# Kernel tuning notes

Hardware: AMD Instinct MI355X
Metric: run time of the kernel (lower is better)

## Reference

```python
import jax, jax.numpy as jnp
import numpy as np

BS, NC, CN, DN = 8, 1024, 64, 64
GH, GW = 32, 32
ALPHA, BPC = 4, 4
G = 8
IN_LO, IN_HI = 0, ALPHA
OUT_LO, OUT_HI = ALPHA, 2 * ALPHA
B_LO, B_HI = 2 * ALPHA, 2 * ALPHA + BPC
HS, HM, HMOD = 256, 256, 128
MOD_IN = 3 * DN + 2 + BPC
MOD_OUT = DN + BPC


def setup_inputs():
    key = jax.random.key(0)
    ks = iter(jax.random.split(key, 40))
    def nrm(shape, s=0.05):
        return jax.random.normal(next(ks), shape, dtype=jnp.float32) * s
    return {
        "x": nrm((BS, NC * DN), 1.0),
        "h": nrm((BS, NC, CN, DN), 0.01),
        "msg": nrm((BS, NC, CN, DN), 0.1),
        "W": nrm((BS, NC, CN, CN), 0.1),
        "decay_logit": jnp.zeros((BS, NC, CN), jnp.float32),
        "cell_context": jnp.zeros((BS, NC, DN), jnp.float32),
        "border_gate_logit": jnp.zeros((BS, NC, BPC), jnp.float32),
        "neuron_id": nrm((NC, CN, DN), 0.02),
        "state_w1": nrm((HS, 2 * DN)), "state_b1": jnp.zeros((HS,), jnp.float32),
        "state_gs1": jnp.ones((G, HS), jnp.float32), "state_gb1": jnp.zeros((G, HS), jnp.float32),
        "state_w2": nrm((DN, HS)), "state_b2": jnp.zeros((DN,), jnp.float32),
        "state_gs2": jnp.ones((G, DN), jnp.float32), "state_gb2": jnp.zeros((G, DN), jnp.float32),
        "msg_w1": nrm((HM, DN)), "msg_b1": jnp.zeros((HM,), jnp.float32),
        "msg_gs1": jnp.ones((G, HM), jnp.float32), "msg_gb1": jnp.zeros((G, HM), jnp.float32),
        "msg_w2": nrm((DN, HM)), "msg_b2": jnp.zeros((DN,), jnp.float32),
        "msg_gs2": jnp.ones((G, DN), jnp.float32), "msg_gb2": jnp.zeros((G, DN), jnp.float32),
        "inject_w": nrm((G, ALPHA * DN, DN)), "inject_b": jnp.zeros((G, ALPHA * DN), jnp.float32),
        "mod_w1": nrm((NC, MOD_IN, HMOD)), "mod_b1": jnp.zeros((NC, HMOD), jnp.float32),
        "mod_w2": nrm((NC, HMOD, MOD_OUT), 0.01), "mod_b2": jnp.zeros((NC, MOD_OUT), jnp.float32),
        "cell_to_group": jnp.arange(NC, dtype=jnp.int32) % G,
    }


def _grouped_mlp(x, c2g, w1, b1, gs1, gb1, w2, b2, gs2, gb2):
    # x: [B, NC, CN, F]; group-specific affine modulation after each linear.
    hid = jnp.einsum('bcnf,hf->bcnh', x, w1) + b1
    hid = jnp.tanh(hid * gs1[c2g][None, :, None, :] + gb1[c2g][None, :, None, :])
    out = jnp.einsum('bcnh,dh->bcnd', hid, w2) + b2
    return jnp.tanh(out * gs2[c2g][None, :, None, :] + gb2[c2g][None, :, None, :])


def reference(x, h, msg, W, decay_logit, cell_context, border_gate_logit, neuron_id,
              state_w1, state_b1, state_gs1, state_gb1, state_w2, state_b2, state_gs2, state_gb2,
              msg_w1, msg_b1, msg_gs1, msg_gb1, msg_w2, msg_b2, msg_gs2, msg_gb2,
              inject_w, inject_b, mod_w1, mod_b1, mod_w2, mod_b2, cell_to_group):
    c2g = cell_to_group
    # 1) dense message passing inside each cell: received = W @ msg
    received = jnp.einsum('bcnm,bcmd->bcnd', W, msg)
    # 2) inject external input into input ports (per-group orthogonal-init projections)
    cell_slice = x.reshape(BS, NC, DN)
    iw, ib = inject_w[c2g], inject_b[c2g]                      # [NC, alpha*DN, DN], [NC, alpha*DN]
    inject = jnp.einsum('bni,noi->bno', cell_slice, iw) + ib   # [BS, NC, alpha*DN]
    received = received.at[:, :, IN_LO:IN_HI].add(inject.reshape(BS, NC, ALPHA, DN))
    # 3) fixed geometric border exchange between neighboring grid cells
    border = msg[:, :, B_LO:B_HI].reshape(BS, GH, GW, BPC, DN)
    incoming = jnp.zeros_like(border)
    incoming = incoming.at[:, 1:, :, 0].set(border[:, :-1, :, 1])
    incoming = incoming.at[:, :-1, :, 1].set(border[:, 1:, :, 0])
    incoming = incoming.at[:, :, 1:, 2].set(border[:, :, :-1, 3])
    incoming = incoming.at[:, :, :-1, 3].set(border[:, :, 1:, 2])
    incoming = incoming.reshape(BS, NC, BPC, DN)
    border_gate = jax.nn.sigmoid(border_gate_logit)[..., None]
    received = received.at[:, :, B_LO:B_HI].add(border_gate * incoming)
    # 4) gated recurrent state update
    decay = jax.nn.sigmoid(decay_logit)[..., None]
    cand = _grouped_mlp(jnp.concatenate([received, h], axis=-1), c2g,
                        state_w1, state_b1, state_gs1, state_gb1,
                        state_w2, state_b2, state_gs2, state_gb2)
    h_new = decay * h + (1.0 - decay) * cand
    # 5) emit new messages (+ per-neuron identity embedding)
    msg_new = _grouped_mlp(h_new, c2g, msg_w1, msg_b1, msg_gs1, msg_gb1,
                           msg_w2, msg_b2, msg_gs2, msg_gb2) + neuron_id[None]
    # 6) readout from output ports
    readout = (msg_new[:, :, OUT_LO:OUT_HI].sum(axis=2) * (ALPHA ** -0.5)).reshape(BS, -1)
    # 7) per-cell modulation MLP (distinct weights per cell)
    h_mean = h_new.mean(axis=2)
    msg_mean = msg_new.mean(axis=2)
    W_row = jnp.abs(W).mean(axis=-1).mean(axis=2, keepdims=True)
    decay_mean = decay_logit.mean(axis=2, keepdims=True)
    feats = jnp.concatenate([h_mean, msg_mean, W_row, decay_mean,
                             cell_context, border_gate_logit], axis=-1)   # [BS, NC, MOD_IN]
    hid = jnp.tanh(jnp.einsum('bcf,cfh->bch', feats, mod_w1) + mod_b1)
    mod = jnp.einsum('bch,cho->bco', hid, mod_w2) + mod_b2                 # [BS, NC, MOD_OUT]
    cell_context_new = cell_context + mod[..., :DN]
    border_gate_logit_new = border_gate_logit + mod[..., DN:]
    return readout, h_new, msg_new, cell_context_new, border_gate_logit_new
```

## Files before the change

### kernel.cpp

```cpp
#include <hip/hip_runtime.h>

#define NCC 1024
#define MODIN 198
#define MODOUT 68
#define HMODL 128

typedef __attribute__((ext_vector_type(8))) short s8v;
typedef __attribute__((ext_vector_type(4))) float f4v;
typedef unsigned short ushort_t;
typedef unsigned int uint_t;

#define OFF_SW1 0
#define OFF_SW2 32768
#define OFF_MW1 49152
#define OFF_MW2 65536
#define FEATS_BYTE_OFF 262144

__device__ __forceinline__ float fast_tanh(float x) {
    const float e = __builtin_amdgcn_exp2f(x * 2.885390081777927f);
    const float r = __builtin_amdgcn_rcpf(e + 1.f);
    return fmaf(-2.f, r, 1.f);
}
__device__ __forceinline__ float fast_sigmoid(float x) {
    const float e = __builtin_amdgcn_exp2f(x * -1.4426950408889634f);
    return __builtin_amdgcn_rcpf(e + 1.f);
}
__device__ __forceinline__ ushort_t f2bf(float x) {
    uint_t u = __builtin_bit_cast(uint_t, x);
    u += 0x7FFFu + ((u >> 16) & 1u);
    return (ushort_t)(u >> 16);
}
__device__ __forceinline__ uint_t pk2(float a, float b) {
    return (uint_t)f2bf(a) | ((uint_t)f2bf(b) << 16);
}
#define SWZ(byteoff, row) ((byteoff) ^ (((row) & 7) << 4))

__global__ __launch_bounds__(256)
void mg_cvtw(const float* __restrict__ sw1, const float* __restrict__ sw2,
             const float* __restrict__ mw1, const float* __restrict__ mw2,
             ushort_t* __restrict__ o) {
    const int i = blockIdx.x * 256 + threadIdx.x;
    float v;
    if (i < 32768)      v = sw1[i];
    else if (i < 49152) v = sw2[i - 32768];
    else if (i < 65536) v = mw1[i - 49152];
    else                v = mw2[i - 65536];
    o[i] = f2bf(v);
}

__global__ __launch_bounds__(256, 4)
void mg_inject(const float* __restrict__ xp, const float* __restrict__ iw,
               const float* __restrict__ ibias, const int* __restrict__ c2g,
               float* __restrict__ injb) {
    const int c = blockIdx.x, t = threadIdx.x;
    const int g = c2g[c];
    __shared__ float s_x[8][64];
    for (int idx = t; idx < 512; idx += 256)
        s_x[idx >> 6][idx & 63] = xp[(size_t)(idx >> 6) * (NCC * 64) + c * 64 + (idx & 63)];
    __syncthreads();
    const float* wrow = iw + (size_t)g * 16384 + t * 64;
    float a0 = 0.f, a1 = 0.f, a2 = 0.f, a3 = 0.f, a4 = 0.f, a5 = 0.f, a6 = 0.f, a7 = 0.f;
    #pragma unroll
    for (int i = 0; i < 64; i += 4) {
        const float4 w4 = *(const float4*)(wrow + i);
        const float4 x0 = *(const float4*)&s_x[0][i];
        const float4 x1 = *(const float4*)&s_x[1][i];
        const float4 x2 = *(const float4*)&s_x[2][i];
        const float4 x3 = *(const float4*)&s_x[3][i];
        const float4 x4 = *(const float4*)&s_x[4][i];
        const float4 x5 = *(const float4*)&s_x[5][i];
        const float4 x6 = *(const float4*)&s_x[6][i];
        const float4 x7 = *(const float4*)&s_x[7][i];
        a0 = fmaf(w4.x, x0.x, a0); a0 = fmaf(w4.y, x0.y, a0); a0 = fmaf(w4.z, x0.z, a0); a0 = fmaf(w4.w, x0.w, a0);
        a1 = fmaf(w4.x, x1.x, a1); a1 = fmaf(w4.y, x1.y, a1); a1 = fmaf(w4.z, x1.z, a1); a1 = fmaf(w4.w, x1.w, a1);
        a2 = fmaf(w4.x, x2.x, a2); a2 = fmaf(w4.y, x2.y, a2); a2 = fmaf(w4.z, x2.z, a2); a2 = fmaf(w4.w, x2.w, a2);
        a3 = fmaf(w4.x, x3.x, a3); a3 = fmaf(w4.y, x3.y, a3); a3 = fmaf(w4.z, x3.z, a3); a3 = fmaf(w4.w, x3.w, a3);
        a4 = fmaf(w4.x, x4.x, a4); a4 = fmaf(w4.y, x4.y, a4); a4 = fmaf(w4.z, x4.z, a4); a4 = fmaf(w4.w, x4.w, a4);
        a5 = fmaf(w4.x, x5.x, a5); a5 = fmaf(w4.y, x5.y, a5); a5 = fmaf(w4.z, x5.z, a5); a5 = fmaf(w4.w, x5.w, a5);
        a6 = fmaf(w4.x, x6.x, a6); a6 = fmaf(w4.y, x6.y, a6); a6 = fmaf(w4.z, x6.z, a6); a6 = fmaf(w4.w, x6.w, a6);
        a7 = fmaf(w4.x, x7.x, a7); a7 = fmaf(w4.y, x7.y, a7); a7 = fmaf(w4.z, x7.z, a7); a7 = fmaf(w4.w, x7.w, a7);
    }
    const float bv = ibias[g * 256 + t];
    const float acc[8] = {a0, a1, a2, a3, a4, a5, a6, a7};
    #pragma unroll
    for (int b = 0; b < 8; b++)
        injb[((size_t)b * NCC + c) * 4096 + t] = acc[b] + bv;
}

__global__ __launch_bounds__(512, 4)
void mg_cell_kernel(
    const float* __restrict__ hp,   const float* __restrict__ msgp,
    const float* __restrict__ Wp,   const float* __restrict__ decayp,
    const float* __restrict__ bglp, const float* __restrict__ nidp,
    const float* __restrict__ sb1,  const float* __restrict__ sgs1,
    const float* __restrict__ sgb1, const float* __restrict__ sb2,
    const float* __restrict__ sgs2, const float* __restrict__ sgb2,
    const float* __restrict__ mb1,  const float* __restrict__ mgs1,
    const float* __restrict__ mgb1, const float* __restrict__ mb2,
    const float* __restrict__ mgs2, const float* __restrict__ mgb2,
    const int*   __restrict__ c2g,  const ushort_t* __restrict__ wb,
    float* __restrict__ out_read, float* __restrict__ out_h,
    float* __restrict__ out_msg,  float* __restrict__ wsf)
{
    const int t  = threadIdx.x;
    const int bc = blockIdx.x;
    const int b  = bc >> 10, c = bc & 1023;
    const int gh = c >> 5, gwc = c & 31;
    const int lane = t & 63, w = t >> 6;
    const int cl = lane & 15, q = lane >> 4;
    const int g  = c2g[c];
    const size_t tile = (size_t)bc * 4096;

    __shared__ ushort_t sHid[16384];
    __shared__ ushort_t sIn[8192];
    __shared__ float s_scr[256];
    __shared__ float s_dec[64];
    __shared__ float s_wsum[8];
    __shared__ float s_dsum;

    ushort_t* sW    = sHid;
    ushort_t* sMsgT = sHid + 4096;

    {
        const int n = t >> 3, m0 = (t & 7) * 8;
        const float* src = Wp + tile + n * 64 + m0;
        const float4 v0 = *(const float4*)(src);
        const float4 v1 = *(const float4*)(src + 4);
        float wsum = fabsf(v0.x) + fabsf(v0.y) + fabsf(v0.z) + fabsf(v0.w)
                   + fabsf(v1.x) + fabsf(v1.y) + fabsf(v1.z) + fabsf(v1.w);
        *(uint_t*)((char*)sW + SWZ(n * 128 + (m0 + 0) * 2, n)) = pk2(v0.x, v0.y);
        *(uint_t*)((char*)sW + SWZ(n * 128 + (m0 + 2) * 2, n)) = pk2(v0.z, v0.w);
        *(uint_t*)((char*)sW + SWZ(n * 128 + (m0 + 4) * 2, n)) = pk2(v1.x, v1.y);
        *(uint_t*)((char*)sW + SWZ(n * 128 + (m0 + 6) * 2, n)) = pk2(v1.z, v1.w);
        #pragma unroll
        for (int off = 32; off > 0; off >>= 1) wsum += __shfl_down(wsum, off);
        if (lane == 0) s_wsum[w] = wsum;
    }
    #pragma unroll
    for (int i = 0; i < 2; i++) {
        const int m = (t >> 4) + i * 32, d0 = (t & 15) * 4;
        const float4 v = *(const float4*)(msgp + tile + (size_t)m * 64 + d0);
        *(ushort_t*)((char*)sMsgT + SWZ((d0 + 0) * 128 + m * 2, d0 + 0)) = f2bf(v.x);
        *(ushort_t*)((char*)sMsgT + SWZ((d0 + 1) * 128 + m * 2, d0 + 1)) = f2bf(v.y);
        *(ushort_t*)((char*)sMsgT + SWZ((d0 + 2) * 128 + m * 2, d0 + 2)) = f2bf(v.z);
        *(ushort_t*)((char*)sMsgT + SWZ((d0 + 3) * 128 + m * 2, d0 + 3)) = f2bf(v.w);
    }
    #pragma unroll
    for (int i = 0; i < 2; i++) {
        const int n = (t >> 4) + i * 32, d0 = (t & 15) * 4;
        const float4 v = *(const float4*)(hp + tile + (size_t)n * 64 + d0);
        *(uint_t*)((char*)sIn + SWZ(n * 256 + (64 + d0) * 2, n))     = pk2(v.x, v.y);
        *(uint_t*)((char*)sIn + SWZ(n * 256 + (64 + d0 + 2) * 2, n)) = pk2(v.z, v.w);
    }
    if (t < 256) {
        const int p = w, dd = lane;
        int ok, nc2, qq;
        if      (p == 0) { ok = (gh > 0);   nc2 = c - 32; qq = 1; }
        else if (p == 1) { ok = (gh < 31);  nc2 = c + 32; qq = 0; }
        else if (p == 2) { ok = (gwc > 0);  nc2 = c - 1;  qq = 3; }
        else             { ok = (gwc < 31); nc2 = c + 1;  qq = 2; }
        float v = 0.f;
        if (ok) v = msgp[((size_t)b * NCC + nc2) * 4096 + (8 + qq) * 64 + dd];
        s_scr[p * 64 + dd] = fast_sigmoid(bglp[(size_t)bc * 4 + p]) * v;
    }
    if (w == 4) {
        const float dl = decayp[(size_t)bc * 64 + lane];
        s_dec[lane] = fast_sigmoid(dl);
        float v = dl;
        #pragma unroll
        for (int off = 32; off > 0; off >>= 1) v += __shfl_down(v, off);
        if (lane == 0) s_dsum = v;
    }
    __syncthreads();

    const f4v fzero = {0.f, 0.f, 0.f, 0.f};
    const int d  = 16 * (w & 3) + cl;
    const int rh = w >> 2;

    {
        f4v wm[2] = {fzero, fzero};
        float injv[4] = {0.f, 0.f, 0.f, 0.f};
        if (rh == 0 && q == 0) {
            #pragma unroll
            for (int r = 0; r < 4; r++) injv[r] = out_h[tile + r * 64 + d];
        }
        __builtin_amdgcn_s_setprio(1);
        #pragma unroll
        for (int ks = 0; ks < 2; ks++) {
            const int k0 = ks * 32 + q * 8;
            const s8v bf = *(const s8v*)((const char*)sMsgT + SWZ(d * 128 + k0 * 2, d));
            #pragma unroll
            for (int rt2 = 0; rt2 < 2; rt2++) {
                const int ar = (rh * 2 + rt2) * 16 + cl;
                const s8v af = *(const s8v*)((const char*)sW + SWZ(ar * 128 + k0 * 2, ar));
                wm[rt2] = __builtin_amdgcn_mfma_f32_16x16x32_bf16(af, bf, wm[rt2], 0, 0, 0);
            }
        }
        __builtin_amdgcn_s_setprio(0);
        #pragma unroll
        for (int rt2 = 0; rt2 < 2; rt2++)
            #pragma unroll
            for (int r = 0; r < 4; r++) {
                const int n = (rh * 2 + rt2) * 16 + q * 4 + r;
                float v = wm[rt2][r];
                if (n < 4)                 v += injv[r];
                else if (n >= 8 && n < 12) v += s_scr[(n - 8) * 64 + d];
                *(ushort_t*)((char*)sIn + SWZ(n * 256 + d * 2, n)) = f2bf(v);
            }
    }
    __syncthreads();

    {
        f4v acc[4][2];
        #pragma unroll
        for (int i = 0; i < 4; i++) { acc[i][0] = fzero; acc[i][1] = fzero; }
        const ushort_t* wb1 = wb + OFF_SW1;
        __builtin_amdgcn_s_setprio(1);
        #pragma unroll
        for (int ks = 0; ks < 4; ks++) {
            const int k0 = ks * 32 + q * 8;
            const s8v bf0 = *(const s8v*)(wb1 + (size_t)(32 * w + 0 * 16 + cl) * 128 + k0);
            const s8v bf1 = *(const s8v*)(wb1 + (size_t)(32 * w + 1 * 16 + cl) * 128 + k0);
            #pragma unroll
            for (int rt = 0; rt < 4; rt++) {
                const int ar = rt * 16 + cl;
                const s8v af = *(const s8v*)((const char*)sIn + SWZ(ar * 256 + k0 * 2, ar));
                acc[rt][0] = __builtin_amdgcn_mfma_f32_16x16x32_bf16(af, bf0, acc[rt][0], 0, 0, 0);
                acc[rt][1] = __builtin_amdgcn_mfma_f32_16x16x32_bf16(af, bf1, acc[rt][1], 0, 0, 0);
            }
        }
        __builtin_amdgcn_s_setprio(0);
        #pragma unroll
        for (int ct2 = 0; ct2 < 2; ct2++) {
            const int hcol = 32 * w + ct2 * 16 + cl;
            const float b1 = sb1[hcol], g1 = sgs1[g * 256 + hcol], o1 = sgb1[g * 256 + hcol];
            #pragma unroll
            for (int rt = 0; rt < 4; rt++)
                #pragma unroll
                for (int r = 0; r < 4; r++) {
                    const int n = rt * 16 + q * 4 + r;
                    const float vv = fast_tanh(fmaf(acc[rt][ct2][r] + b1, g1, o1));
                    *(ushort_t*)((char*)sHid + SWZ(n * 512 + hcol * 2, n)) = f2bf(vv);
                }
        }
    }
    __syncthreads();

    {
        f4v a2[2][2];
        a2[0][0] = fzero; a2[0][1] = fzero; a2[1][0] = fzero; a2[1][1] = fzero;
        const ushort_t* wb2 = wb + OFF_SW2;
        __builtin_amdgcn_s_setprio(1);
        #pragma unroll
        for (int ks = 0; ks < 8; ks++) {
            const int k0 = ks * 32 + q * 8;
            const s8v bf = *(const s8v*)(wb2 + (size_t)d * 256 + k0);
            #pragma unroll
            for (int rt2 = 0; rt2 < 2; rt2++) {
                const int ar = (rh * 2 + rt2) * 16 + cl;
                const s8v af = *(const s8v*)((const char*)sHid + SWZ(ar * 512 + k0 * 2, ar));
                a2[rt2][ks & 1] = __builtin_amdgcn_mfma_f32_16x16x32_bf16(af, bf, a2[rt2][ks & 1], 0, 0, 0);
            }
        }
        __builtin_amdgcn_s_setprio(0);
        const float b2 = sb2[d], g2 = sgs2[g * 64 + d], o2 = sgb2[g * 64 + d];
        float hsum = 0.f;
        #pragma unroll
        for (int rt2 = 0; rt2 < 2; rt2++)
            #pragma unroll
            for (int r = 0; r < 4; r++) {
                const int n = (rh * 2 + rt2) * 16 + q * 4 + r;
                const float cand = fast_tanh(fmaf(a2[rt2][0][r] + a2[rt2][1][r] + b2, g2, o2));
                const ushort_t hu = *(const ushort_t*)((const char*)sIn + SWZ(n * 256 + (64 + d) * 2, n));
                const float hv = __builtin_bit_cast(float, (uint_t)hu << 16);
                const float hn = fmaf(s_dec[n], hv - cand, cand);
                out_h[tile + (size_t)n * 64 + d] = hn;
                *(ushort_t*)((char*)sIn + SWZ(n * 256 + d * 2, n)) = f2bf(hn);
                hsum += hn;
            }
        hsum += __shfl_xor(hsum, 16);
        hsum += __shfl_xor(hsum, 32);
        if (q == 0) s_scr[rh * 64 + d] = hsum;
    }
    __syncthreads();

    {
        f4v acc[4][2];
        #pragma unroll
        for (int i = 0; i < 4; i++) { acc[i][0] = fzero; acc[i][1] = fzero; }
        const ushort_t* wm1 = wb + OFF_MW1;
        __builtin_amdgcn_s_setprio(1);
        #pragma unroll
        for (int ks = 0; ks < 2; ks++) {
            const int k0 = ks * 32 + q * 8;
            const s8v bf0 = *(const s8v*)(wm1 + (size_t)(32 * w + 0 * 16 + cl) * 64 + k0);
            const s8v bf1 = *(const s8v*)(wm1 + (size_t)(32 * w + 1 * 16 + cl) * 64 + k0);
            #pragma unroll
            for (int rt = 0; rt < 4; rt++) {
                const int ar = rt * 16 + cl;
                const s8v af = *(const s8v*)((const char*)sIn + SWZ(ar * 256 + k0 * 2, ar));
                acc[rt][0] = __builtin_amdgcn_mfma_f32_16x16x32_bf16(af, bf0, acc[rt][0], 0, 0, 0);
                acc[rt][1] = __builtin_amdgcn_mfma_f32_16x16x32_bf16(af, bf1, acc[rt][1], 0, 0, 0);
            }
        }
        __builtin_amdgcn_s_setprio(0);
        #pragma unroll
        for (int ct2 = 0; ct2 < 2; ct2++) {
            const int hcol = 32 * w + ct2 * 16 + cl;
            const float b1 = mb1[hcol], g1 = mgs1[g * 256 + hcol], o1 = mgb1[g * 256 + hcol];
            #pragma unroll
            for (int rt = 0; rt < 4; rt++)
                #pragma unroll
                for (int r = 0; r < 4; r++) {
                    const int n = rt * 16 + q * 4 + r;
                    const float vv = fast_tanh(fmaf(acc[rt][ct2][r] + b1, g1, o1));
                    *(ushort_t*)((char*)sHid + SWZ(n * 512 + hcol * 2, n)) = f2bf(vv);
                }
        }
    }
    __syncthreads();

    {
        float nv[8];
        #pragma unroll
        for (int rt2 = 0; rt2 < 2; rt2++)
            #pragma unroll
            for (int r = 0; r < 4; r++) {
                const int n = (rh * 2 + rt2) * 16 + q * 4 + r;
                nv[rt2 * 4 + r] = nidp[(size_t)c * 4096 + (size_t)n * 64 + d];
            }
        f4v a6[2][2];
        a6[0][0] = fzero; a6[0][1] = fzero; a6[1][0] = fzero; a6[1][1] = fzero;
        const ushort_t* wm2 = wb + OFF_MW2;
        __builtin_amdgcn_s_setprio(1);
        #pragma unroll
        for (int ks = 0; ks < 8; ks++) {
            const int k0 = ks * 32 + q * 8;
            const s8v bf = *(const s8v*)(wm2 + (size_t)d * 256 + k0);
            #pragma unroll
            for (int rt2 = 0; rt2 < 2; rt2++) {
                const int ar = (rh * 2 + rt2) * 16 + cl;
                const s8v af = *(const s8v*)((const char*)sHid + SWZ(ar * 512 + k0 * 2, ar));
                a6[rt2][ks & 1] = __builtin_amdgcn_mfma_f32_16x16x32_bf16(af, bf, a6[rt2][ks & 1], 0, 0, 0);
            }
        }
        __builtin_amdgcn_s_setprio(0);
        const float b2 = mb2[d], g2 = mgs2[g * 64 + d], o2 = mgb2[g * 64 + d];
        float msum = 0.f, ro = 0.f;
        #pragma unroll
        for (int rt2 = 0; rt2 < 2; rt2++)
            #pragma unroll
            for (int r = 0; r < 4; r++) {
                const int n = (rh * 2 + rt2) * 16 + q * 4 + r;
                const float mv = fast_tanh(fmaf(a6[rt2][0][r] + a6[rt2][1][r] + b2, g2, o2))
                                 + nv[rt2 * 4 + r];
                out_msg[tile + (size_t)n * 64 + d] = mv;
                msum += mv;
                if (rt2 == 0 && q == 1 && rh == 0) ro += mv;
            }
        msum += __shfl_xor(msum, 16);
        msum += __shfl_xor(msum, 32);
        if (q == 0) s_scr[128 + rh * 64 + d] = msum;
        if (rh == 0 && q == 1) out_read[((size_t)b * NCC + c) * 64 + d] = ro * 0.5f;
    }
    __syncthreads();

    if (t < 132) {
        float v = 0.f;
        if (t < 64)        v = (s_scr[t] + s_scr[64 + t]) * (1.f / 64.f);
        else if (t < 128)  v = (s_scr[64 + t] + s_scr[128 + t]) * (1.f / 64.f);
        else if (t == 128) v = (s_wsum[0] + s_wsum[1] + s_wsum[2] + s_wsum[3]
                              + s_wsum[4] + s_wsum[5] + s_wsum[6] + s_wsum[7]) * (1.f / 4096.f);
        else if (t == 129) v = s_dsum * (1.f / 64.f);
        wsf[(size_t)bc * 132 + t] = v;
    }
}

__global__ __launch_bounds__(256, 2)
void mg_mod_kernel(
    const float* __restrict__ wsf,   const float* __restrict__ modw1,
    const float* __restrict__ modb1, const float* __restrict__ modw2,
    const float* __restrict__ modb2, const float* __restrict__ ctxp,
    const float* __restrict__ bglp,  float* __restrict__ out_ctx,
    float* __restrict__ out_bg)
{
    const int c = blockIdx.x;
    const int t = threadIdx.x;
    __shared__ float s_f[8][MODIN];
    __shared__ float s_h2[8][HMODL];

    for (int k = t; k < 8 * MODIN; k += 256) {
        const int b = k / MODIN, f = k - b * MODIN;
        float v;
        if (f < 130)      v = wsf[((size_t)b * NCC + c) * 132 + f];
        else if (f < 194) v = ctxp[((size_t)b * NCC + c) * 64 + (f - 130)];
        else              v = bglp[((size_t)b * NCC + c) * 4 + (f - 194)];
        s_f[b][f] = v;
    }
    __syncthreads();

    {
        const int hh = t & 127, bh = (t >> 7) * 4;
        float a0 = 0.f, a1 = 0.f, a2 = 0.f, a3 = 0.f;
        const float* wp = modw1 + (size_t)c * MODIN * HMODL + hh;
        for (int f = 0; f < MODIN; f++) {
            const float wv = wp[(size_t)f * HMODL];
            a0 = fmaf(s_f[bh + 0][f], wv, a0);
            a1 = fmaf(s_f[bh + 1][f], wv, a1);
            a2 = fmaf(s_f[bh + 2][f], wv, a2);
            a3 = fmaf(s_f[bh + 3][f], wv, a3);
        }
        const float bv = modb1[(size_t)c * HMODL + hh];
        s_h2[bh + 0][hh] = fast_tanh(a0 + bv);
        s_h2[bh + 1][hh] = fast_tanh(a1 + bv);
        s_h2[bh + 2][hh] = fast_tanh(a2 + bv);
        s_h2[bh + 3][hh] = fast_tanh(a3 + bv);
    }
    __syncthreads();

    for (int idx = t; idx < 8 * MODOUT; idx += 256) {
        const int b = idx / MODOUT, o = idx - b * MODOUT;
        float acc = modb2[(size_t)c * MODOUT + o];
        const float* wp = modw2 + (size_t)c * HMODL * MODOUT + o;
        const float* hrow = s_h2[b];
        for (int hh = 0; hh < HMODL; hh++)
            acc = fmaf(hrow[hh], wp[(size_t)hh * MODOUT], acc);
        if (o < 64)
            out_ctx[((size_t)b * NCC + c) * 64 + o] =
                ctxp[((size_t)b * NCC + c) * 64 + o] + acc;
        else
            out_bg[((size_t)b * NCC + c) * 4 + (o - 64)] =
                bglp[((size_t)b * NCC + c) * 4 + (o - 64)] + acc;
    }
}

extern "C" void kernel_launch(void* const* d_in, const int* in_sizes, int n_in,
                              void* d_out, int out_size, void* d_ws, size_t ws_size,
                              hipStream_t stream) {
    const float* xp     = (const float*)d_in[0];
    const float* hp     = (const float*)d_in[1];
    const float* msgp   = (const float*)d_in[2];
    const float* Wp     = (const float*)d_in[3];
    const float* decayp = (const float*)d_in[4];
    const float* ctxp   = (const float*)d_in[5];
    const float* bglp   = (const float*)d_in[6];
    const float* nidp   = (const float*)d_in[7];
    const float* sw1    = (const float*)d_in[8];
    const float* sb1    = (const float*)d_in[9];
    const float* sgs1   = (const float*)d_in[10];
    const float* sgb1   = (const float*)d_in[11];
    const float* sw2    = (const float*)d_in[12];
    const float* sb2    = (const float*)d_in[13];
    const float* sgs2   = (const float*)d_in[14];
    const float* sgb2   = (const float*)d_in[15];
    const float* mw1    = (const float*)d_in[16];
    const float* mb1    = (const float*)d_in[17];
    const float* mgs1   = (const float*)d_in[18];
    const float* mgb1   = (const float*)d_in[19];
    const float* mw2    = (const float*)d_in[20];
    const float* mb2    = (const float*)d_in[21];
    const float* mgs2   = (const float*)d_in[22];
    const float* mgb2   = (const float*)d_in[23];
    const float* iw     = (const float*)d_in[24];
    const float* ibias  = (const float*)d_in[25];
    const float* modw1  = (const float*)d_in[26];
    const float* modb1  = (const float*)d_in[27];
    const float* modw2  = (const float*)d_in[28];
    const float* modb2  = (const float*)d_in[29];
    const int*   c2g    = (const int*)d_in[30];

    float* out      = (float*)d_out;
    float* out_read = out;
    float* out_h    = out_read + 524288;
    float* out_msg  = out_h + 33554432;
    float* out_ctx  = out_msg + 33554432;
    float* out_bg   = out_ctx + 524288;

    ushort_t* wb  = (ushort_t*)d_ws;
    float*    wsf = (float*)((char*)d_ws + FEATS_BYTE_OFF);

    mg_cvtw<<<320, 256, 0, stream>>>(sw1, sw2, mw1, mw2, wb);

    mg_inject<<<1024, 256, 0, stream>>>(xp, iw, ibias, c2g, out_h);

    mg_cell_kernel<<<8192, 512, 0, stream>>>(
        hp, msgp, Wp, decayp, bglp, nidp,
        sb1, sgs1, sgb1, sb2, sgs2, sgb2,
        mb1, mgs1, mgb1, mb2, mgs2, mgb2,
        c2g, wb, out_read, out_h, out_msg, wsf);

    mg_mod_kernel<<<1024, 256, 0, stream>>>(
        wsf, modw1, modb1, modw2, modb2, ctxp, bglp, out_ctx, out_bg);
}
```

Baseline: 469.9 us.

## Double cell-kernel block to 1024 threads and halve per-wave MFMA tiles

The per-cell kernel now launches 1024 threads (16 waves) per tile instead of 512. Each wave handles one 16-row or 16-column MFMA tile instead of two, and loads a single float4 per thread. The partial-sum scratch for the h and msg means and the W-abs sums are widened to cover 16 waves. The aim is more waves per tile to hide latency, at the cost of less instruction-level parallelism per wave. The new launch bound (1024, 8) may also force a tight register budget and cause spills.

Measured after the change: 692.5 us. +47.4%, slower.

```diff
diff --git a/kernel.cpp b/kernel.cpp
--- a/kernel.cpp
+++ b/kernel.cpp
@@ -87,7 +87,7 @@
         injb[((size_t)b * NCC + c) * 4096 + t] = acc[b] + bv;
 }
 
-__global__ __launch_bounds__(512, 4)
+__global__ __launch_bounds__(1024, 8)
 void mg_cell_kernel(
     const float* __restrict__ hp,   const float* __restrict__ msgp,
     const float* __restrict__ Wp,   const float* __restrict__ decayp,
@@ -113,41 +113,34 @@
 
     __shared__ ushort_t sHid[16384];
     __shared__ ushort_t sIn[8192];
-    __shared__ float s_scr[256];
+    __shared__ float s_scr[512];
     __shared__ float s_dec[64];
-    __shared__ float s_wsum[8];
+    __shared__ float s_wsum[16];
     __shared__ float s_dsum;
 
     ushort_t* sW    = sHid;
     ushort_t* sMsgT = sHid + 4096;
 
     {
-        const int n = t >> 3, m0 = (t & 7) * 8;
-        const float* src = Wp + tile + n * 64 + m0;
-        const float4 v0 = *(const float4*)(src);
-        const float4 v1 = *(const float4*)(src + 4);
-        float wsum = fabsf(v0.x) + fabsf(v0.y) + fabsf(v0.z) + fabsf(v0.w)
-                   + fabsf(v1.x) + fabsf(v1.y) + fabsf(v1.z) + fabsf(v1.w);
-        *(uint_t*)((char*)sW + SWZ(n * 128 + (m0 + 0) * 2, n)) = pk2(v0.x, v0.y);
-        *(uint_t*)((char*)sW + SWZ(n * 128 + (m0 + 2) * 2, n)) = pk2(v0.z, v0.w);
-        *(uint_t*)((char*)sW + SWZ(n * 128 + (m0 + 4) * 2, n)) = pk2(v1.x, v1.y);
-        *(uint_t*)((char*)sW + SWZ(n * 128 + (m0 + 6) * 2, n)) = pk2(v1.z, v1.w);
+        const int n = t >> 4, m0 = (t & 15) * 4;
+        const float4 v = *(const float4*)(Wp + tile + (size_t)n * 64 + m0);
+        float wsum = fabsf(v.x) + fabsf(v.y) + fabsf(v.z) + fabsf(v.w);
+        *(uint_t*)((char*)sW + SWZ(n * 128 + (m0 + 0) * 2, n)) = pk2(v.x, v.y);
+        *(uint_t*)((char*)sW + SWZ(n * 128 + (m0 + 2) * 2, n)) = pk2(v.z, v.w);
         #pragma unroll
         for (int off = 32; off > 0; off >>= 1) wsum += __shfl_down(wsum, off);
         if (lane == 0) s_wsum[w] = wsum;
     }
-    #pragma unroll
-    for (int i = 0; i < 2; i++) {
-        const int m = (t >> 4) + i * 32, d0 = (t & 15) * 4;
+    {
+        const int m = t >> 4, d0 = (t & 15) * 4;
         const float4 v = *(const float4*)(msgp + tile + (size_t)m * 64 + d0);
         *(ushort_t*)((char*)sMsgT + SWZ((d0 + 0) * 128 + m * 2, d0 + 0)) = f2bf(v.x);
         *(ushort_t*)((char*)sMsgT + SWZ((d0 + 1) * 128 + m * 2, d0 + 1)) = f2bf(v.y);
         *(ushort_t*)((char*)sMsgT + SWZ((d0 + 2) * 128 + m * 2, d0 + 2)) = f2bf(v.z);
         *(ushort_t*)((char*)sMsgT + SWZ((d0 + 3) * 128 + m * 2, d0 + 3)) = f2bf(v.w);
     }
-    #pragma unroll
-    for (int i = 0; i < 2; i++) {
-        const int n = (t >> 4) + i * 32, d0 = (t & 15) * 4;
+    {
+        const int n = t >> 4, d0 = (t & 15) * 4;
         const float4 v = *(const float4*)(hp + tile + (size_t)n * 64 + d0);
         *(uint_t*)((char*)sIn + SWZ(n * 256 + (64 + d0) * 2, n))     = pk2(v.x, v.y);
         *(uint_t*)((char*)sIn + SWZ(n * 256 + (64 + d0 + 2) * 2, n)) = pk2(v.z, v.w);
@@ -178,7 +171,7 @@
     const int rh = w >> 2;
 
     {
-        f4v wm[2] = {fzero, fzero};
+        f4v wm = fzero;
         float injv[4] = {0.f, 0.f, 0.f, 0.f};
         if (rh == 0 && q == 0) {
             #pragma unroll
@@ -189,95 +182,77 @@
         for (int ks = 0; ks < 2; ks++) {
             const int k0 = ks * 32 + q * 8;
             const s8v bf = *(const s8v*)((const char*)sMsgT + SWZ(d * 128 + k0 * 2, d));
-            #pragma unroll
-            for (int rt2 = 0; rt2 < 2; rt2++) {
-                const int ar = (rh * 2 + rt2) * 16 + cl;
-                const s8v af = *(const s8v*)((const char*)sW + SWZ(ar * 128 + k0 * 2, ar));
-                wm[rt2] = __builtin_amdgcn_mfma_f32_16x16x32_bf16(af, bf, wm[rt2], 0, 0, 0);
-            }
+            const int ar = rh * 16 + cl;
+            const s8v af = *(const s8v*)((const char*)sW + SWZ(ar * 128 + k0 * 2, ar));
+            wm = __builtin_amdgcn_mfma_f32_16x16x32_bf16(af, bf, wm, 0, 0, 0);
         }
         __builtin_amdgcn_s_setprio(0);
         #pragma unroll
-        for (int rt2 = 0; rt2 < 2; rt2++)
-            #pragma unroll
-            for (int r = 0; r < 4; r++) {
-                const int n = (rh * 2 + rt2) * 16 + q * 4 + r;
-                float v = wm[rt2][r];
-                if (n < 4)                 v += injv[r];
-                else if (n >= 8 && n < 12) v += s_scr[(n - 8) * 64 + d];
-                *(ushort_t*)((char*)sIn + SWZ(n * 256 + d * 2, n)) = f2bf(v);
-            }
-    }
-    __syncthreads();
-
-    {
-        f4v acc[4][2];
-        #pragma unroll
-        for (int i = 0; i < 4; i++) { acc[i][0] = fzero; acc[i][1] = fzero; }
+        for (int r = 0; r < 4; r++) {
+            const int n = rh * 16 + q * 4 + r;
+            float v = wm[r];
+            if (n < 4)                 v += injv[r];
+            else if (n >= 8 && n < 12) v += s_scr[(n - 8) * 64 + d];
+            *(ushort_t*)((char*)sIn + SWZ(n * 256 + d * 2, n)) = f2bf(v);
+        }
+    }
+    __syncthreads();
+
+    {
+        f4v acc[4] = {fzero, fzero, fzero, fzero};
         const ushort_t* wb1 = wb + OFF_SW1;
+        const int hcol = 16 * w + cl;
         __builtin_amdgcn_s_setprio(1);
         #pragma unroll
         for (int ks = 0; ks < 4; ks++) {
             const int k0 = ks * 32 + q * 8;
-            const s8v bf0 = *(const s8v*)(wb1 + (size_t)(32 * w + 0 * 16 + cl) * 128 + k0);
-            const s8v bf1 = *(const s8v*)(wb1 + (size_t)(32 * w + 1 * 16 + cl) * 128 + k0);
+            const s8v bf = *(const s8v*)(wb1 + (size_t)hcol * 128 + k0);
             #pragma unroll
             for (int rt = 0; rt < 4; rt++) {
                 const int ar = rt * 16 + cl;
                 const s8v af = *(const s8v*)((const char*)sIn + SWZ(ar * 256 + k0 * 2, ar));
-                acc[rt][0] = __builtin_amdgcn_mfma_f32_16x16x32_bf16(af, bf0, acc[rt][0], 0, 0, 0);
-                acc[rt][1] = __builtin_amdgcn_mfma_f32_16x16x32_bf16(af, bf1, acc[rt][1], 0, 0, 0);
+                acc[rt] = __builtin_amdgcn_mfma_f32_16x16x32_bf16(af, bf, acc[rt], 0, 0, 0);
             }
         }
         __builtin_amdgcn_s_setprio(0);
-        #pragma unroll
-        for (int ct2 = 0; ct2 < 2; ct2++) {
-            const int hcol = 32 * w + ct2 * 16 + cl;
-            const float b1 = sb1[hcol], g1 = sgs1[g * 256 + hcol], o1 = sgb1[g * 256 + hcol];
-            #pragma unroll
-            for (int rt = 0; rt < 4; rt++)
-                #pragma unroll
-                for (int r = 0; r < 4; r++) {
-                    const int n = rt * 16 + q * 4 + r;
-                    const float vv = fast_tanh(fmaf(acc[rt][ct2][r] + b1, g1, o1));
-                    *(ushort_t*)((char*)sHid + SWZ(n * 512 + hcol * 2, n)) = f2bf(vv);
-                }
-        }
-    }
-    __syncthreads();
-
-    {
-        f4v a2[2][2];
-        a2[0][0] = fzero; a2[0][1] = fzero; a2[1][0] = fzero; a2[1][1] = fzero;
+        const float b1 = sb1[hcol], g1 = sgs1[g * 256 + hcol], o1 = sgb1[g * 256 + hcol];
+        #pragma unroll
+        for (int rt = 0; rt < 4; rt++)
+            #pragma unroll
+            for (int r = 0; r < 4; r++) {
+                const int n = rt * 16 + q * 4 + r;
+                const float vv = fast_tanh(fmaf(acc[rt][r] + b1, g1, o1));
+                *(ushort_t*)((char*)sHid + SWZ(n * 512 + hcol * 2, n)) = f2bf(vv);
+            }
+    }
+    __syncthreads();
+
+    {
+        f4v a2[2] = {fzero, fzero};
         const ushort_t* wb2 = wb + OFF_SW2;
         __builtin_amdgcn_s_setprio(1);
         #pragma unroll
         for (int ks = 0; ks < 8; ks++) {
             const int k0 = ks * 32 + q * 8;
             const s8v bf = *(const s8v*)(wb2 + (size_t)d * 256 + k0);
-            #pragma unroll
-            for (int rt2 = 0; rt2 < 2; rt2++) {
-                const int ar = (rh * 2 + rt2) * 16 + cl;
-                const s8v af = *(const s8v*)((const char*)sHid + SWZ(ar * 512 + k0 * 2, ar));
-                a2[rt2][ks & 1] = __builtin_amdgcn_mfma_f32_16x16x32_bf16(af, bf, a2[rt2][ks & 1], 0, 0, 0);
-            }
+            const int ar = rh * 16 + cl;
+            const s8v af = *(const s8v*)((const char*)sHid + SWZ(ar * 512 + k0 * 2, ar));
+            a2[ks & 1] = __builtin_amdgcn_mfma_f32_16x16x32_bf16(af, bf, a2[ks & 1], 0, 0, 0);
         }
         __builtin_amdgcn_s_setprio(0);
         const float b2 = sb2[d], g2 = sgs2[g * 64 + d], o2 = sgb2[g * 64 + d];
         float hsum = 0.f;
         #pragma unroll
-        for (int rt2 = 0; rt2 < 2; rt2++)
-            #pragma unroll
-            for (int r = 0; r < 4; r++) {
-                const int n = (rh * 2 + rt2) * 16 + q * 4 + r;
-                const float cand = fast_tanh(fmaf(a2[rt2][0][r] + a2[rt2][1][r] + b2, g2, o2));
-                const ushort_t hu = *(const ushort_t*)((const char*)sIn + SWZ(n * 256 + (64 + d) * 2, n));
-                const float hv = __builtin_bit_cast(float, (uint_t)hu << 16);
-                const float hn = fmaf(s_dec[n], hv - cand, cand);
-                out_h[tile + (size_t)n * 64 + d] = hn;
-                *(ushort_t*)((char*)sIn + SWZ(n * 256 + d * 2, n)) = f2bf(hn);
-                hsum += hn;
-            }
+        for (int r = 0; r < 4; r++) {
+            const int n = rh * 16 + q * 4 + r;
+            const float cand = fast_tanh(fmaf(a2[0][r] + a2[1][r] + b2, g2, o2));
+            const ushort_t hu = *(const ushort_t*)((const char*)sIn + SWZ(n * 256 + (64 + d) * 2, n));
+            const float hv = __builtin_bit_cast(float, (uint_t)hu << 16);
+            const float hn = fmaf(s_dec[n], hv - cand, cand);
+            out_h[tile + (size_t)n * 64 + d] = hn;
+            *(ushort_t*)((char*)sIn + SWZ(n * 256 + d * 2, n)) = f2bf(hn);
+            hsum += hn;
+        }
         hsum += __shfl_xor(hsum, 16);
         hsum += __shfl_xor(hsum, 32);
         if (q == 0) s_scr[rh * 64 + d] = hsum;
@@ -285,93 +260,83 @@
     __syncthreads();
 
     {
-        f4v acc[4][2];
-        #pragma unroll
-        for (int i = 0; i < 4; i++) { acc[i][0] = fzero; acc[i][1] = fzero; }
+        f4v acc[4] = {fzero, fzero, fzero, fzero};
         const ushort_t* wm1 = wb + OFF_MW1;
+        const int hcol = 16 * w + cl;
         __builtin_amdgcn_s_setprio(1);
         #pragma unroll
         for (int ks = 0; ks < 2; ks++) {
             const int k0 = ks * 32 + q * 8;
-            const s8v bf0 = *(const s8v*)(wm1 + (size_t)(32 * w + 0 * 16 + cl) * 64 + k0);
-            const s8v bf1 = *(const s8v*)(wm1 + (size_t)(32 * w + 1 * 16 + cl) * 64 + k0);
+            const s8v bf = *(const s8v*)(wm1 + (size_t)hcol * 64 + k0);
             #pragma unroll
             for (int rt = 0; rt < 4; rt++) {
                 const int ar = rt * 16 + cl;
                 const s8v af = *(const s8v*)((const char*)sIn + SWZ(ar * 256 + k0 * 2, ar));
-                acc[rt][0] = __builtin_amdgcn_mfma_f32_16x16x32_bf16(af, bf0, acc[rt][0], 0, 0, 0);
-                acc[rt][1] = __builtin_amdgcn_mfma_f32_16x16x32_bf16(af, bf1, acc[rt][1], 0, 0, 0);
+                acc[rt] = __builtin_amdgcn_mfma_f32_16x16x32_bf16(af, bf, acc[rt], 0, 0, 0);
             }
         }
         __builtin_amdgcn_s_setprio(0);
-        #pragma unroll
-        for (int ct2 = 0; ct2 < 2; ct2++) {
-            const int hcol = 32 * w + ct2 * 16 + cl;
-            const float b1 = mb1[hcol], g1 = mgs1[g * 256 + hcol], o1 = mgb1[g * 256 + hcol];
-            #pragma unroll
-            for (int rt = 0; rt < 4; rt++)
-                #pragma unroll
-                for (int r = 0; r < 4; r++) {
-                    const int n = rt * 16 + q * 4 + r;
-                    const float vv = fast_tanh(fmaf(acc[rt][ct2][r] + b1, g1, o1));
-                    *(ushort_t*)((char*)sHid + SWZ(n * 512 + hcol * 2, n)) = f2bf(vv);
-                }
-        }
-    }
-    __syncthreads();
-
-    {
-        float nv[8];
-        #pragma unroll
-        for (int rt2 = 0; rt2 < 2; rt2++)
+        const float b1 = mb1[hcol], g1 = mgs1[g * 256 + hcol], o1 = mgb1[g * 256 + hcol];
+        #pragma unroll
+        for (int rt = 0; rt < 4; rt++)
             #pragma unroll
             for (int r = 0; r < 4; r++) {
-                const int n = (rh * 2 + rt2) * 16 + q * 4 + r;
-                nv[rt2 * 4 + r] = nidp[(size_t)c * 4096 + (size_t)n * 64 + d];
+                const int n = rt * 16 + q * 4 + r;
+                const float vv = fast_tanh(fmaf(acc[rt][r] + b1, g1, o1));
+                *(ushort_t*)((char*)sHid + SWZ(n * 512 + hcol * 2, n)) = f2bf(vv);
             }
-        f4v a6[2][2];
-        a6[0][0] = fzero; a6[0][1] = fzero; a6[1][0] = fzero; a6[1][1] = fzero;
+    }
+    __syncthreads();
+
+    {
+        float nv[4];
+        #pragma unroll
+        for (int r = 0; r < 4; r++) {
+            const int n = rh * 16 + q * 4 + r;
+            nv[r] = nidp[(size_t)c * 4096 + (size_t)n * 64 + d];
+        }
+        f4v a6[2] = {fzero, fzero};
         const ushort_t* wm2 = wb + OFF_MW2;
         __builtin_amdgcn_s_setprio(1);
         #pragma unroll
         for (int ks = 0; ks < 8; ks++) {
             const int k0 = ks * 32 + q * 8;
             const s8v bf = *(const s8v*)(wm2 + (size_t)d * 256 + k0);
-            #pragma unroll
-            for (int rt2 = 0; rt2 < 2; rt2++) {
-                const int ar = (rh * 2 + rt2) * 16 + cl;
-                const s8v af = *(const s8v*)((const char*)sHid + SWZ(ar * 512 + k0 * 2, ar));
-                a6[rt2][ks & 1] = __builtin_amdgcn_mfma_f32_16x16x32_bf16(af, bf, a6[rt2][ks & 1], 0, 0, 0);
-            }
+            const int ar = rh * 16 + cl;
+            const s8v af = *(const s8v*)((const char*)sHid + SWZ(ar * 512 + k0 * 2, ar));
+            a6[ks & 1] = __builtin_amdgcn_mfma_f32_16x16x32_bf16(af, bf, a6[ks & 1], 0, 0, 0);
         }
         __builtin_amdgcn_s_setprio(0);
         const float b2 = mb2[d], g2 = mgs2[g * 64 + d], o2 = mgb2[g * 64 + d];
         float msum = 0.f, ro = 0.f;
         #pragma unroll
-        for (int rt2 = 0; rt2 < 2; rt2++)
-            #pragma unroll
-            for (int r = 0; r < 4; r++) {
-                const int n = (rh * 2 + rt2) * 16 + q * 4 + r;
-                const float mv = fast_tanh(fmaf(a6[rt2][0][r] + a6[rt2][1][r] + b2, g2, o2))
-                                 + nv[rt2 * 4 + r];
-                out_msg[tile + (size_t)n * 64 + d] = mv;
-                msum += mv;
-                if (rt2 == 0 && q == 1 && rh == 0) ro += mv;
-            }
+        for (int r = 0; r < 4; r++) {
+            const int n = rh * 16 + q * 4 + r;
+            const float mv = fast_tanh(fmaf(a6[0][r] + a6[1][r] + b2, g2, o2)) + nv[r];
+            out_msg[tile + (size_t)n * 64 + d] = mv;
+            msum += mv;
+            ro += mv;
+        }
         msum += __shfl_xor(msum, 16);
         msum += __shfl_xor(msum, 32);
-        if (q == 0) s_scr[128 + rh * 64 + d] = msum;
+        if (q == 0) s_scr[256 + rh * 64 + d] = msum;
         if (rh == 0 && q == 1) out_read[((size_t)b * NCC + c) * 64 + d] = ro * 0.5f;
     }
     __syncthreads();
 
     if (t < 132) {
         float v = 0.f;
-        if (t < 64)        v = (s_scr[t] + s_scr[64 + t]) * (1.f / 64.f);
-        else if (t < 128)  v = (s_scr[64 + t] + s_scr[128 + t]) * (1.f / 64.f);
-        else if (t == 128) v = (s_wsum[0] + s_wsum[1] + s_wsum[2] + s_wsum[3]
-                              + s_wsum[4] + s_wsum[5] + s_wsum[6] + s_wsum[7]) * (1.f / 4096.f);
-        else if (t == 129) v = s_dsum * (1.f / 64.f);
+        if (t < 64) {
+            v = (s_scr[t] + s_scr[64 + t] + s_scr[128 + t] + s_scr[192 + t]) * (1.f / 64.f);
+        } else if (t < 128) {
+            const int dd = t - 64;
+            v = (s_scr[256 + dd] + s_scr[320 + dd] + s_scr[384 + dd] + s_scr[448 + dd]) * (1.f / 64.f);
+        } else if (t == 128) {
+            float s = 0.f;
+            #pragma unroll
+            for (int ww = 0; ww < 16; ww++) s += s_wsum[ww];
+            v = s * (1.f / 4096.f);
+        } else if (t == 129) v = s_dsum * (1.f / 64.f);
         wsf[(size_t)bc * 132 + t] = v;
     }
 }
@@ -483,7 +448,7 @@
 
     mg_inject<<<1024, 256, 0, stream>>>(xp, iw, ibias, c2g, out_h);
 
-    mg_cell_kernel<<<8192, 512, 0, stream>>>(
+    mg_cell_kernel<<<8192, 1024, 0, stream>>>(
         hp, msgp, Wp, decayp, bglp, nidp,
         sb1, sgs1, sgb1, sb2, sgs2, sgb2,
         mb1, mgs1, mgb1, mb2, mgs2, mgb2,
```

## Split hidden dimension into two halves to halve shared-memory hidden buffer

Applied to the files above, without the earlier changes.

Both grouped MLPs now compute the 256-wide hidden layer in two 128-column passes. Each pass's second-layer partial product is accumulated before the next half is written. This halves the sHid LDS buffer (32KB to 16KB) and the per-thread first-layer accumulators, which is meant to raise occupancy, i.e. more resident blocks per CU. In exchange it adds extra __syncthreads barriers and serializes the two halves within a block.

Measured after the change: 465.5 us. No clear change (-0.9%).

```diff
diff --git a/kernel.cpp b/kernel.cpp
--- a/kernel.cpp
+++ b/kernel.cpp
@@ -111,7 +111,7 @@
     const int g  = c2g[c];
     const size_t tile = (size_t)bc * 4096;
 
-    __shared__ ushort_t sHid[16384];
+    __shared__ ushort_t sHid[8192];
     __shared__ ushort_t sIn[8192];
     __shared__ float s_scr[256];
     __shared__ float s_dec[64];
@@ -211,58 +211,57 @@
     __syncthreads();
 
     {
-        f4v acc[4][2];
-        #pragma unroll
-        for (int i = 0; i < 4; i++) { acc[i][0] = fzero; acc[i][1] = fzero; }
-        const ushort_t* wb1 = wb + OFF_SW1;
-        __builtin_amdgcn_s_setprio(1);
-        #pragma unroll
-        for (int ks = 0; ks < 4; ks++) {
-            const int k0 = ks * 32 + q * 8;
-            const s8v bf0 = *(const s8v*)(wb1 + (size_t)(32 * w + 0 * 16 + cl) * 128 + k0);
-            const s8v bf1 = *(const s8v*)(wb1 + (size_t)(32 * w + 1 * 16 + cl) * 128 + k0);
-            #pragma unroll
-            for (int rt = 0; rt < 4; rt++) {
-                const int ar = rt * 16 + cl;
-                const s8v af = *(const s8v*)((const char*)sIn + SWZ(ar * 256 + k0 * 2, ar));
-                acc[rt][0] = __builtin_amdgcn_mfma_f32_16x16x32_bf16(af, bf0, acc[rt][0], 0, 0, 0);
-                acc[rt][1] = __builtin_amdgcn_mfma_f32_16x16x32_bf16(af, bf1, acc[rt][1], 0, 0, 0);
-            }
-        }
-        __builtin_amdgcn_s_setprio(0);
-        #pragma unroll
-        for (int ct2 = 0; ct2 < 2; ct2++) {
-            const int hcol = 32 * w + ct2 * 16 + cl;
-            const float b1 = sb1[hcol], g1 = sgs1[g * 256 + hcol], o1 = sgb1[g * 256 + hcol];
-            #pragma unroll
-            for (int rt = 0; rt < 4; rt++)
-                #pragma unroll
-                for (int r = 0; r < 4; r++) {
-                    const int n = rt * 16 + q * 4 + r;
-                    const float vv = fast_tanh(fmaf(acc[rt][ct2][r] + b1, g1, o1));
-                    *(ushort_t*)((char*)sHid + SWZ(n * 512 + hcol * 2, n)) = f2bf(vv);
-                }
-        }
-    }
-    __syncthreads();
-
-    {
         f4v a2[2][2];
         a2[0][0] = fzero; a2[0][1] = fzero; a2[1][0] = fzero; a2[1][1] = fzero;
+        const ushort_t* wb1 = wb + OFF_SW1;
         const ushort_t* wb2 = wb + OFF_SW2;
-        __builtin_amdgcn_s_setprio(1);
-        #pragma unroll
-        for (int ks = 0; ks < 8; ks++) {
-            const int k0 = ks * 32 + q * 8;
-            const s8v bf = *(const s8v*)(wb2 + (size_t)d * 256 + k0);
-            #pragma unroll
-            for (int rt2 = 0; rt2 < 2; rt2++) {
-                const int ar = (rh * 2 + rt2) * 16 + cl;
-                const s8v af = *(const s8v*)((const char*)sHid + SWZ(ar * 512 + k0 * 2, ar));
-                a2[rt2][ks & 1] = __builtin_amdgcn_mfma_f32_16x16x32_bf16(af, bf, a2[rt2][ks & 1], 0, 0, 0);
-            }
+        #pragma unroll
+        for (int p = 0; p < 2; p++) {
+            {
+                f4v acc[4] = {fzero, fzero, fzero, fzero};
+                const int lc = 16 * w + cl;
+                const int hcol = p * 128 + lc;
+                __builtin_amdgcn_s_setprio(1);
+                #pragma unroll
+                for (int ks = 0; ks < 4; ks++) {
+                    const int k0 = ks * 32 + q * 8;
+                    const s8v bf = *(const s8v*)(wb1 + (size_t)hcol * 128 + k0);
+                    #pragma unroll
+                    for (int rt = 0; rt < 4; rt++) {
+                        const int ar = rt * 16 + cl;
+                        const s8v af = *(const s8v*)((const char*)sIn + SWZ(ar * 256 + k0 * 2, ar));
+                        acc[rt] = __builtin_amdgcn_mfma_f32_16x16x32_bf16(af, bf, acc[rt], 0, 0, 0);
+                    }
+                }
+                __builtin_amdgcn_s_setprio(0);
+                const float b1 = sb1[hcol], g1 = sgs1[g * 256 + hcol], o1 = sgb1[g * 256 + hcol];
+                #pragma unroll
+                for (int rt = 0; rt < 4; rt++)
+                    #pragma unroll
+                    for (int r = 0; r < 4; r++) {
+                        const int n = rt * 16 + q * 4 + r;
+                        const float vv = fast_tanh(fmaf(acc[rt][r] + b1, g1, o1));
+                        *(ushort_t*)((char*)sHid + SWZ(n * 256 + lc * 2, n)) = f2bf(vv);
+                    }
+            }
+            __syncthreads();
+            {
+                __builtin_amdgcn_s_setprio(1);
+                #pragma unroll
+                for (int ks = 0; ks < 4; ks++) {
+                    const int k0 = ks * 32 + q * 8;
+                    const s8v bf = *(const s8v*)(wb2 + (size_t)d * 256 + p * 128 + k0);
+                    #pragma unroll
+                    for (int rt2 = 0; rt2 < 2; rt2++) {
+                        const int ar = (rh * 2 + rt2) * 16 + cl;
+                        const s8v af = *(const s8v*)((const char*)sHid + SWZ(ar * 256 + k0 * 2, ar));
+                        a2[rt2][ks & 1] = __builtin_amdgcn_mfma_f32_16x16x32_bf16(af, bf, a2[rt2][ks & 1], 0, 0, 0);
+                    }
+                }
+                __builtin_amdgcn_s_setprio(0);
+            }
+            if (p == 0) __syncthreads();
         }
-        __builtin_amdgcn_s_setprio(0);
         const float b2 = sb2[d], g2 = sgs2[g * 64 + d], o2 = sgb2[g * 64 + d];
         float hsum = 0.f;
         #pragma unroll
@@ -285,42 +284,6 @@
     __syncthreads();
 
     {
-        f4v acc[4][2];
-        #pragma unroll
-        for (int i = 0; i < 4; i++) { acc[i][0] = fzero; acc[i][1] = fzero; }
-        const ushort_t* wm1 = wb + OFF_MW1;
-        __builtin_amdgcn_s_setprio(1);
-        #pragma unroll
-        for (int ks = 0; ks < 2; ks++) {
-            const int k0 = ks * 32 + q * 8;
-            const s8v bf0 = *(const s8v*)(wm1 + (size_t)(32 * w + 0 * 16 + cl) * 64 + k0);
-            const s8v bf1 = *(const s8v*)(wm1 + (size_t)(32 * w + 1 * 16 + cl) * 64 + k0);
-            #pragma unroll
-            for (int rt = 0; rt < 4; rt++) {
-                const int ar = rt * 16 + cl;
-                const s8v af = *(const s8v*)((const char*)sIn + SWZ(ar * 256 + k0 * 2, ar));
-                acc[rt][0] = __builtin_amdgcn_mfma_f32_16x16x32_bf16(af, bf0, acc[rt][0], 0, 0, 0);
-                acc[rt][1] = __builtin_amdgcn_mfma_f32_16x16x32_bf16(af, bf1, acc[rt][1], 0, 0, 0);
-            }
-        }
-        __builtin_amdgcn_s_setprio(0);
-        #pragma unroll
-        for (int ct2 = 0; ct2 < 2; ct2++) {
-            const int hcol = 32 * w + ct2 * 16 + cl;
-            const float b1 = mb1[hcol], g1 = mgs1[g * 256 + hcol], o1 = mgb1[g * 256 + hcol];
-            #pragma unroll
-            for (int rt = 0; rt < 4; rt++)
-                #pragma unroll
-                for (int r = 0; r < 4; r++) {
-                    const int n = rt * 16 + q * 4 + r;
-                    const float vv = fast_tanh(fmaf(acc[rt][ct2][r] + b1, g1, o1));
-                    *(ushort_t*)((char*)sHid + SWZ(n * 512 + hcol * 2, n)) = f2bf(vv);
-                }
-        }
-    }
-    __syncthreads();
-
-    {
         float nv[8];
         #pragma unroll
         for (int rt2 = 0; rt2 < 2; rt2++)
@@ -331,20 +294,55 @@
             }
         f4v a6[2][2];
         a6[0][0] = fzero; a6[0][1] = fzero; a6[1][0] = fzero; a6[1][1] = fzero;
+        const ushort_t* wm1 = wb + OFF_MW1;
         const ushort_t* wm2 = wb + OFF_MW2;
-        __builtin_amdgcn_s_setprio(1);
-        #pragma unroll
-        for (int ks = 0; ks < 8; ks++) {
-            const int k0 = ks * 32 + q * 8;
-            const s8v bf = *(const s8v*)(wm2 + (size_t)d * 256 + k0);
-            #pragma unroll
-            for (int rt2 = 0; rt2 < 2; rt2++) {
-                const int ar = (rh * 2 + rt2) * 16 + cl;
-                const s8v af = *(const s8v*)((const char*)sHid + SWZ(ar * 512 + k0 * 2, ar));
-                a6[rt2][ks & 1] = __builtin_amdgcn_mfma_f32_16x16x32_bf16(af, bf, a6[rt2][ks & 1], 0, 0, 0);
-            }
+        #pragma unroll
+        for (int p = 0; p < 2; p++) {
+            {
+                f4v acc[4] = {fzero, fzero, fzero, fzero};
+                const int lc = 16 * w + cl;
+                const int hcol = p * 128 + lc;
+                __builtin_amdgcn_s_setprio(1);
+                #pragma unroll
+                for (int ks = 0; ks < 2; ks++) {
+                    const int k0 = ks * 32 + q * 8;
+                    const s8v bf = *(const s8v*)(wm1 + (size_t)hcol * 64 + k0);
+                    #pragma unroll
+                    for (int rt = 0; rt < 4; rt++) {
+                        const int ar = rt * 16 + cl;
+                        const s8v af = *(const s8v*)((const char*)sIn + SWZ(ar * 256 + k0 * 2, ar));
+                        acc[rt] = __builtin_amdgcn_mfma_f32_16x16x32_bf16(af, bf, acc[rt], 0, 0, 0);
+                    }
+                }
+                __builtin_amdgcn_s_setprio(0);
+                const float b1 = mb1[hcol], g1 = mgs1[g * 256 + hcol], o1 = mgb1[g * 256 + hcol];
+                #pragma unroll
+                for (int rt = 0; rt < 4; rt++)
+                    #pragma unroll
+                    for (int r = 0; r < 4; r++) {
+                        const int n = rt * 16 + q * 4 + r;
+                        const float vv = fast_tanh(fmaf(acc[rt][r] + b1, g1, o1));
+                        *(ushort_t*)((char*)sHid + SWZ(n * 256 + lc * 2, n)) = f2bf(vv);
+                    }
+            }
+            __syncthreads();
+            {
+                __builtin_amdgcn_s_setprio(1);
+                #pragma unroll
+                for (int ks = 0; ks < 4; ks++) {
+                    const int k0 = ks * 32 + q * 8;
+                    const s8v bf = *(const s8v*)(wm2 + (size_t)d * 256 + p * 128 + k0);
+                    #pragma unroll
+                    for (int rt2 = 0; rt2 < 2; rt2++) {
+                        const int ar = (rh * 2 + rt2) * 16 + cl;
+                        const s8v af = *(const s8v*)((const char*)sHid + SWZ(ar * 256 + k0 * 2, ar));
+                        a6[rt2][ks & 1] = __builtin_amdgcn_mfma_f32_16x16x32_bf16(af, bf, a6[rt2][ks & 1], 0, 0, 0);
+                    }
+                }
+                __builtin_amdgcn_s_setprio(0);
+            }
+            if (p == 0) __syncthreads();
         }
-        __builtin_amdgcn_s_setprio(0);
         const float b2 = mb2[d], g2 = mgs2[g * 64 + d], o2 = mgb2[g * 64 + d];
         float msum = 0.f, ro = 0.f;
         #pragma unroll
```
